# Optimization experiments

Hardware: AMD Instinct MI355X
Metric: run time of the kernel (lower is better)

The kernel has to match this reference:

```python
import jax, jax.numpy as jnp
import numpy as np

N_NODES = 100000


def gcn_conv(x, W, b, src, dst, norm, n_nodes):
    # x: [N, F_in] -> [N, F_out]; GCNConv: D^-1/2 (A+I) D^-1/2 (X W) + b
    h = x @ W                                   # [N, F_out]
    msg = h[src] * norm[:, None]                # [E+N, F_out] gather + scale
    out = jax.ops.segment_sum(msg, dst, num_segments=n_nodes)  # scatter-add
    return out + b


def setup_inputs() -> dict:
    key = jax.random.key(0)
    k0, k1, k2, k3, k4, k5 = jax.random.split(key, 6)
    n, e, f_in, f_hid, n_cls = N_NODES, 1600000, 128, 128, 3
    x = jax.random.normal(k0, (n, f_in), dtype=jnp.float32)
    edge_index = jax.random.randint(k1, (2, e), 0, n, dtype=jnp.int64)
    s1 = 1.0 / np.sqrt(f_in)
    s2 = 1.0 / np.sqrt(f_hid)
    W1 = jax.random.uniform(k2, (f_in, f_hid), jnp.float32, -s1, s1)
    b1 = jnp.zeros((f_hid,), jnp.float32)
    W2 = jax.random.uniform(k3, (f_hid, f_hid), jnp.float32, -s2, s2)
    b2 = jnp.zeros((f_hid,), jnp.float32)
    Wfc = jax.random.uniform(k4, (f_hid, n_cls), jnp.float32, -s2, s2)
    bfc = jax.random.uniform(k5, (n_cls,), jnp.float32, -s2, s2)
    return {"x": x, "edge_index": edge_index, "W1": W1, "b1": b1,
            "W2": W2, "b2": b2, "Wfc": Wfc, "bfc": bfc}


def reference(x, edge_index, W1, b1, W2, b2, Wfc, bfc):
    n = x.shape[0]
    # add self-loops (PyG GCNConv default add_self_loops=True)
    loops = jnp.arange(n, dtype=edge_index.dtype)
    src = jnp.concatenate([edge_index[0], loops])
    dst = jnp.concatenate([edge_index[1], loops])
    deg = jax.ops.segment_sum(jnp.ones_like(dst, dtype=x.dtype), dst,
                              num_segments=n)
    dinv = jax.lax.rsqrt(deg)                   # deg >= 1 due to self-loops
    norm = dinv[src] * dinv[dst]                # [E+N]
    h = jax.nn.relu(gcn_conv(x, W1, b1, src, dst, norm, n))   # dropout=eval id
    h = jax.nn.relu(gcn_conv(h, W2, b2, src, dst, norm, n))
    return jnp.tanh(h @ Wfc + bfc)              # [N, 3]
```

## Files before the change

kernel.cpp:

```cpp
#include <hip/hip_runtime.h>
#include <hip/hip_bf16.h>
#include <hip/hip_fp16.h>


#define NODE_F 128

typedef __attribute__((ext_vector_type(8))) short bf16x8;
typedef __attribute__((ext_vector_type(8))) unsigned short u16x8;
typedef __attribute__((ext_vector_type(4))) float f32x4;

__device__ inline unsigned short bf16_rn(float x) {
    unsigned u = __builtin_bit_cast(unsigned, x);
    unsigned r = (u + 0x7fffu + ((u >> 16) & 1u)) >> 16;
    return (unsigned short)r;
}
__device__ inline float bf16_to_f(unsigned short h) {
    unsigned u = (unsigned)h << 16;
    return __builtin_bit_cast(float, u);
}
__device__ inline void acc8_h(float a[8], uint4 v, float s) {
    unsigned vv[4] = {v.x, v.y, v.z, v.w};
    #pragma unroll
    for (int j = 0; j < 4; ++j) {
        float2 f = __half22float2(__builtin_bit_cast(__half2, vv[j]));
        a[2 * j]     += f.x * s;
        a[2 * j + 1] += f.y * s;
    }
}


__global__ __launch_bounds__(256) void wconv_kernel(const float* __restrict__ W1,
                                                    const float* __restrict__ W2,
                                                    unsigned short* __restrict__ WhiT,
                                                    unsigned short* __restrict__ WloT)
{
    const float* W = blockIdx.x ? W2 : W1;
    unsigned short* hiT = WhiT + blockIdx.x * 128 * 128;
    unsigned short* loT = WloT + blockIdx.x * 128 * 128;
    int tid = threadIdx.x;
    for (int i = tid; i < 128 * 128; i += 256) {
        int k = i >> 7, n = i & 127;
        float x = W[i];
        unsigned short hi = bf16_rn(x);
        float lo = x - bf16_to_f(hi);
        hiT[n * 128 + k] = hi;
        loT[n * 128 + k] = bf16_rn(lo);
    }
}


__global__ __launch_bounds__(256) void scan_block_kernel(
    const int* __restrict__ degE, int* __restrict__ rsA,
    int* __restrict__ bsum, int N)
{
    __shared__ int s[256];
    const int tid = threadIdx.x;
    const int idx = blockIdx.x * 1024 + tid * 4;
    int v0 = (idx + 0 < N) ? degE[idx + 0] : 0;
    int v1 = (idx + 1 < N) ? degE[idx + 1] : 0;
    int v2 = (idx + 2 < N) ? degE[idx + 2] : 0;
    int v3 = (idx + 3 < N) ? degE[idx + 3] : 0;
    int t = v0 + v1 + v2 + v3;
    s[tid] = t;
    __syncthreads();
    #pragma unroll
    for (int off = 1; off < 256; off <<= 1) {
        int x = (tid >= off) ? s[tid - off] : 0;
        __syncthreads();
        s[tid] += x;
        __syncthreads();
    }
    int excl = s[tid] - t;
    if (idx + 0 < N) rsA[idx + 0] = excl;
    if (idx + 1 < N) rsA[idx + 1] = excl + v0;
    if (idx + 2 < N) rsA[idx + 2] = excl + v0 + v1;
    if (idx + 3 < N) rsA[idx + 3] = excl + v0 + v1 + v2;
    if (tid == 255) bsum[blockIdx.x] = s[255];
}

__global__ __launch_bounds__(1024) void scan_tops_kernel(int* __restrict__ bsum, int nb) {
    __shared__ int s[1024];
    const int tid = threadIdx.x;
    int v = (tid < nb) ? bsum[tid] : 0;
    s[tid] = v;
    __syncthreads();
    #pragma unroll
    for (int off = 1; off < 1024; off <<= 1) {
        int x = (tid >= off) ? s[tid - off] : 0;
        __syncthreads();
        s[tid] += x;
        __syncthreads();
    }
    if (tid < nb) bsum[tid] = s[tid] - v;
}


__global__ __launch_bounds__(256) void finish_fill_kernel(
    const int* __restrict__ src, const int* __restrict__ dst,
    const unsigned short* __restrict__ rank,
    const int* __restrict__ rsA, const int* __restrict__ bsum,
    int* __restrict__ rsB, float* __restrict__ dinv,
    const int* __restrict__ degE, int* __restrict__ csr_src,
    int E, int N, int fill_blocks)
{
    if ((int)blockIdx.x < fill_blocks) {
        int e = blockIdx.x * 256 + threadIdx.x;
        if (e < E) {
            int d = dst[e];
            csr_src[rsA[d] + bsum[d >> 10] + (int)rank[e]] = src[e];
        }
    } else {
        int i = (blockIdx.x - fill_blocks) * 256 + threadIdx.x;
        if (i < N) {
            int rs = rsA[i] + bsum[i >> 10];
            rsB[i] = rs;
            dinv[i] = rsqrtf((float)degE[i] + 1.0f);
            if (i == N - 1) rsB[N] = rs + degE[i];
        }
    }
}


template<bool SCALE_OUT>
__device__ __forceinline__ void gemm_compute(
    const unsigned short* __restrict__ WhiT, const unsigned short* __restrict__ WloT,
    const float* __restrict__ dinv, __half* __restrict__ Hout, int N, int rbase,
    unsigned short* xhi, unsigned short* xlo)
{
    const int tid  = threadIdx.x;
    const int lane = tid & 63;
    const int w    = tid >> 6;

    bf16x8 bhi[2][4], blo[2][4];
    {
        int n0   = w * 32 + (lane & 15);
        int koct = (lane >> 4) * 8;
        #pragma unroll
        for (int nt = 0; nt < 2; ++nt) {
            #pragma unroll
            for (int kk = 0; kk < 4; ++kk) {
                size_t o = (size_t)(n0 + nt * 16) * 128 + kk * 32 + koct;
                bhi[nt][kk] = *reinterpret_cast<const bf16x8*>(WhiT + o);
                blo[nt][kk] = *reinterpret_cast<const bf16x8*>(WloT + o);
            }
        }
    }

    f32x4 acc[4][2];
    #pragma unroll
    for (int m = 0; m < 4; ++m)
        #pragma unroll
        for (int nt = 0; nt < 2; ++nt)
            acc[m][nt] = (f32x4){0.f, 0.f, 0.f, 0.f};

    #pragma unroll
    for (int kk = 0; kk < 4; ++kk) {
        #pragma unroll
        for (int m = 0; m < 4; ++m) {
            int row  = m * 16 + (lane & 15);
            int koff = kk * 64 + (lane >> 4) * 16;
            int byte = row * 256 + (koff ^ ((row & 7) << 4));
            bf16x8 ahi = *reinterpret_cast<const bf16x8*>(reinterpret_cast<char*>(xhi) + byte);
            bf16x8 alo = *reinterpret_cast<const bf16x8*>(reinterpret_cast<char*>(xlo) + byte);
            #pragma unroll
            for (int nt = 0; nt < 2; ++nt) {
                acc[m][nt] = __builtin_amdgcn_mfma_f32_16x16x32_bf16(ahi, bhi[nt][kk], acc[m][nt], 0, 0, 0);
                acc[m][nt] = __builtin_amdgcn_mfma_f32_16x16x32_bf16(ahi, blo[nt][kk], acc[m][nt], 0, 0, 0);
                acc[m][nt] = __builtin_amdgcn_mfma_f32_16x16x32_bf16(alo, bhi[nt][kk], acc[m][nt], 0, 0, 0);
            }
        }
    }

    #pragma unroll
    for (int m = 0; m < 4; ++m) {
        int row = rbase + m * 16 + (lane >> 4) * 4;
        int col = w * 32 + (lane & 15);
        #pragma unroll
        for (int nt = 0; nt < 2; ++nt) {
            #pragma unroll
            for (int r = 0; r < 4; ++r) {
                if (row + r < N) {
                    float v = acc[m][nt][r];
                    if (SCALE_OUT) v *= dinv[row + r];
                    Hout[(size_t)(row + r) * NODE_F + col + nt * 16] = __float2half(v);
                }
            }
        }
    }
}


__device__ __forceinline__ void gemm1_body(
    const float* __restrict__ Xf,
    const unsigned short* __restrict__ WhiT, const unsigned short* __restrict__ WloT,
    __half* __restrict__ Hout, int N, int bid,
    unsigned short* xhi, unsigned short* xlo)
{
    const int tid   = threadIdx.x;
    const int rbase = bid * 64;

    #pragma unroll
    for (int it = 0; it < 8; ++it) {
        int f   = it * 256 + tid;
        int row = f >> 5;
        int k4  = f & 31;
        float4 v = make_float4(0.f, 0.f, 0.f, 0.f);
        if (rbase + row < N)
            v = *reinterpret_cast<const float4*>(Xf + (size_t)(rbase + row) * NODE_F + k4 * 4);
        float xs[4] = {v.x, v.y, v.z, v.w};
        ushort4 h4, l4;
        unsigned short* hp = &h4.x;
        unsigned short* lp = &l4.x;
        #pragma unroll
        for (int j = 0; j < 4; ++j) {
            unsigned short hi = bf16_rn(xs[j]);
            hp[j] = hi;
            lp[j] = bf16_rn(xs[j] - bf16_to_f(hi));
        }
        int byte = row * 256 + ((k4 * 8) ^ ((row & 7) << 4));
        *reinterpret_cast<ushort4*>(reinterpret_cast<char*>(xhi) + byte) = h4;
        *reinterpret_cast<ushort4*>(reinterpret_cast<char*>(xlo) + byte) = l4;
    }
    __syncthreads();
    gemm_compute<false>(WhiT, WloT, nullptr, Hout, N, rbase, xhi, xlo);
}


__global__ __launch_bounds__(256) void gemm1deg_kernel(
    const int* __restrict__ dst, int* __restrict__ degE,
    unsigned short* __restrict__ rank, int E,
    int edge_blocks, int gemm_blocks,
    const float* __restrict__ X, const unsigned short* __restrict__ WhiT,
    const unsigned short* __restrict__ WloT, __half* __restrict__ H, int N)
{
    __shared__ unsigned short xhi[64 * 128];
    __shared__ unsigned short xlo[64 * 128];
    int q = blockIdx.x / 5, r = blockIdx.x % 5;
    if (r == 4) {
        int stride = edge_blocks * 256;
        for (int e = q * 256 + threadIdx.x; e < E; e += stride)
            rank[e] = (unsigned short)atomicAdd(&degE[dst[e]], 1);
    } else {
        int gid = q * 4 + r;
        if (gid < gemm_blocks)
            gemm1_body(X, WhiT, WloT, H, N, gid, xhi, xlo);
    }
}


template<bool EDGE_SCALE>
__device__ __forceinline__ void gather_core(
    const __half* __restrict__ Hs, const int* __restrict__ csr_src,
    const int* __restrict__ row_start, const float* __restrict__ dinv,
    int node, int ql, int qi, float a[8])
{
    const char* Hb = reinterpret_cast<const char*>(Hs);
    #pragma unroll
    for (int j = 0; j < 8; ++j) a[j] = 0.f;
    if (qi == 0) {
        float ds = EDGE_SCALE ? dinv[node] : 1.0f;
        acc8_h(a, *reinterpret_cast<const uint4*>(Hb + ((size_t)node * 256 + ql * 16)), ds);
    }

    int i   = row_start[node];
    int end = row_start[node + 1];
    for (; i + 7 < end; i += 8) {
        int s0 = csr_src[i + qi];
        int s1 = csr_src[i + 4 + qi];
        float d0 = EDGE_SCALE ? dinv[s0] : 1.0f;
        float d1 = EDGE_SCALE ? dinv[s1] : 1.0f;
        uint4 v0 = *reinterpret_cast<const uint4*>(Hb + ((size_t)s0 * 256 + ql * 16));
        uint4 v1 = *reinterpret_cast<const uint4*>(Hb + ((size_t)s1 * 256 + ql * 16));
        acc8_h(a, v0, d0);
        acc8_h(a, v1, d1);
    }
    for (; i < end; i += 4) {
        if (i + qi < end) {
            int s = csr_src[i + qi];
            float ds = EDGE_SCALE ? dinv[s] : 1.0f;
            acc8_h(a, *reinterpret_cast<const uint4*>(Hb + ((size_t)s * 256 + ql * 16)), ds);
        }
    }
    #pragma unroll
    for (int j = 0; j < 8; ++j) {
        a[j] += __shfl_xor(a[j], 32);
        a[j] += __shfl_xor(a[j], 16);
    }
}


__global__ __launch_bounds__(256) void aggemm2_kernel(
    const __half* __restrict__ H, const int* __restrict__ csr_src,
    const int* __restrict__ row_start, const float* __restrict__ dinv,
    const float* __restrict__ b1,
    const unsigned short* __restrict__ WhiT, const unsigned short* __restrict__ WloT,
    __half* __restrict__ H2, int N)
{
    __shared__ unsigned short xhi[64 * 128];
    __shared__ unsigned short xlo[64 * 128];
    const int tid  = threadIdx.x;
    const int lane = tid & 63;
    const int w    = tid >> 6;
    const int ql   = lane & 15, qi = lane >> 4;
    const int rbase = blockIdx.x * 64;

    float bv[8];
    {
        float4 b0 = *reinterpret_cast<const float4*>(b1 + ql * 8);
        float4 b4 = *reinterpret_cast<const float4*>(b1 + ql * 8 + 4);
        bv[0] = b0.x; bv[1] = b0.y; bv[2] = b0.z; bv[3] = b0.w;
        bv[4] = b4.x; bv[5] = b4.y; bv[6] = b4.z; bv[7] = b4.w;
    }

    for (int r16 = 0; r16 < 16; ++r16) {
        int row  = w * 16 + r16;
        int node = rbase + row;
        float a[8];
        if (node < N)
            gather_core<true>(H, csr_src, row_start, dinv, node, ql, qi, a);
        if (qi == 0) {
            u16x8 h8 = {0, 0, 0, 0, 0, 0, 0, 0};
            u16x8 l8 = {0, 0, 0, 0, 0, 0, 0, 0};
            if (node < N) {
                float dd = dinv[node];
                #pragma unroll
                for (int j = 0; j < 8; ++j) {
                    float r = fmaxf(bv[j] + dd * a[j], 0.f);
                    unsigned short hi = bf16_rn(r);
                    h8[j] = hi;
                    l8[j] = bf16_rn(r - bf16_to_f(hi));
                }
            }
            int byte = row * 256 + ((ql * 16) ^ ((row & 7) << 4));
            *reinterpret_cast<u16x8*>(reinterpret_cast<char*>(xhi) + byte) = h8;
            *reinterpret_cast<u16x8*>(reinterpret_cast<char*>(xlo) + byte) = l8;
        }
    }
    __syncthreads();
    gemm_compute<true>(WhiT, WloT, dinv, H2, N, rbase, xhi, xlo);
}


__global__ __launch_bounds__(256) void gather2fc_kernel(
    const __half* __restrict__ Hs, const int* __restrict__ csr_src,
    const int* __restrict__ row_start, const float* __restrict__ dinv,
    const float* __restrict__ b, const float* __restrict__ Wfc,
    const float* __restrict__ bfc, float* __restrict__ out, int N)
{
    int node = (blockIdx.x * blockDim.x + threadIdx.x) >> 6;
    int lane = threadIdx.x & 63;
    int ql = lane & 15, qi = lane >> 4;
    if (node >= N) return;

    float a[8];
    gather_core<false>(Hs, csr_src, row_start, dinv, node, ql, qi, a);

    const float dd = dinv[node];
    float p0 = 0.f, p1 = 0.f, p2 = 0.f;
    #pragma unroll
    for (int j = 0; j < 8; ++j) {
        float r = fmaxf(b[ql * 8 + j] + dd * a[j], 0.f);
        const float* wr = Wfc + (size_t)(ql * 8 + j) * 3;
        p0 += r * wr[0]; p1 += r * wr[1]; p2 += r * wr[2];
    }
    #pragma unroll
    for (int off = 8; off > 0; off >>= 1) {
        p0 += __shfl_down(p0, off);
        p1 += __shfl_down(p1, off);
        p2 += __shfl_down(p2, off);
    }
    if (lane == 0) {
        out[(size_t)node * 3 + 0] = tanhf(p0 + bfc[0]);
        out[(size_t)node * 3 + 1] = tanhf(p1 + bfc[1]);
        out[(size_t)node * 3 + 2] = tanhf(p2 + bfc[2]);
    }
}

extern "C" void kernel_launch(void* const* d_in, const int* in_sizes, int n_in,
                              void* d_out, int out_size, void* d_ws, size_t ws_size,
                              hipStream_t stream)
{
    const float* x    = (const float*)d_in[0];
    const int*   edge = (const int*)d_in[1];
    const float* W1   = (const float*)d_in[2];
    const float* b1   = (const float*)d_in[3];
    const float* W2   = (const float*)d_in[4];
    const float* b2   = (const float*)d_in[5];
    const float* Wfc  = (const float*)d_in[6];
    const float* bfc  = (const float*)d_in[7];
    float* out = (float*)d_out;

    const int N = in_sizes[0] / NODE_F;
    const int E = in_sizes[1] / 2;
    const int* src = edge;
    const int* dst = edge + E;

    char* ws = (char*)d_ws;
    size_t off = 0;
    auto alloc = [&](size_t bytes) {
        void* p = ws + off;
        off += (bytes + 511) & ~511ull;
        return p;
    };
    const int nblk = (N + 1023) / 1024;
    float* dinv      = (float*)alloc((size_t)N * 4);
    int*   degE      = (int*)  alloc((size_t)N * 4);
    unsigned short* rank = (unsigned short*)alloc((size_t)E * 2);
    int*   rsA       = (int*)  alloc((size_t)N * 4);
    int*   rsB       = (int*)  alloc((size_t)(N + 1) * 4);
    int*   bsum      = (int*)  alloc((size_t)nblk * 4);
    int*   csr_src   = (int*)  alloc((size_t)E * 4);
    unsigned short* WhiT = (unsigned short*)alloc(2 * 128 * 128 * 2);
    unsigned short* WloT = (unsigned short*)alloc(2 * 128 * 128 * 2);
    __half* H        = (__half*)alloc((size_t)N * NODE_F * 2);
    __half* H2       = (__half*)alloc((size_t)N * NODE_F * 2);
    (void)ws_size; (void)n_in; (void)out_size;

    const int B = 256;
    const int gemm_grid   = (N + 63) / 64;
    const int gather_grid = (N + 3) / 4;
    const int fill_blocks = (E + B - 1) / B;
    const int fin_blocks  = (N + B - 1) / B;

    const int edge_blocks  = (gemm_grid + 3) / 4;
    const int total_blocks = gemm_grid + edge_blocks + 4;

    wconv_kernel<<<2, B, 0, stream>>>(W1, W2, WhiT, WloT);
    hipMemsetAsync(degE, 0, (size_t)N * 4, stream);

    gemm1deg_kernel<<<total_blocks, B, 0, stream>>>(
        dst, degE, rank, E, edge_blocks, gemm_grid, x, WhiT, WloT, H, N);

    scan_block_kernel<<<nblk, B, 0, stream>>>(degE, rsA, bsum, N);
    scan_tops_kernel<<<1, 1024, 0, stream>>>(bsum, nblk);

    finish_fill_kernel<<<fill_blocks + fin_blocks, B, 0, stream>>>(
        src, dst, rank, rsA, bsum, rsB, dinv, degE, csr_src, E, N, fill_blocks);

    aggemm2_kernel<<<gemm_grid, B, 0, stream>>>(
        H, csr_src, rsB, dinv, b1, WhiT + 128 * 128, WloT + 128 * 128, H2, N);

    gather2fc_kernel<<<gather_grid, B, 0, stream>>>(H2, csr_src, rsB, dinv, b2,
                                                    Wfc, bfc, out, N);
}
```

Baseline: 340.5 us.

## Split fused layer-2 gather+GEMM into separate gather and GEMM kernels

Replaces the fused aggregate-then-GEMM kernel, which ran 16 sequential row gathers per wave before a shared-memory GEMM, with a standalone gather kernel (one node per wave, full grid parallelism) writing fp16 activations to a new buffer, followed by a GEMM kernel that loads those rows into LDS. The aim is to expose far more parallelism and latency hiding for the irregular gather, instead of having the GEMM blocks serialize over gathers. In exchange it adds a global round trip of an N×128 fp16 intermediate, an extra launch, and rounds the hidden activations to fp16 before the bf16 hi/lo split, which loses some precision.

```diff
diff --git a/kernel.cpp b/kernel.cpp
--- a/kernel.cpp
+++ b/kernel.cpp
@@ -289,55 +289,66 @@
 }
 
 
-__global__ __launch_bounds__(256) void aggemm2_kernel(
+__global__ __launch_bounds__(256) void gather1_kernel(
     const __half* __restrict__ H, const int* __restrict__ csr_src,
     const int* __restrict__ row_start, const float* __restrict__ dinv,
-    const float* __restrict__ b1,
+    const float* __restrict__ b, __half* __restrict__ A1, int N)
+{
+    int node = (blockIdx.x * blockDim.x + threadIdx.x) >> 6;
+    int lane = threadIdx.x & 63;
+    int ql = lane & 15, qi = lane >> 4;
+    if (node >= N) return;
+
+    float a[8];
+    gather_core<true>(H, csr_src, row_start, dinv, node, ql, qi, a);
+
+    if (qi == 0) {
+        const float dd = dinv[node];
+        u16x8 o;
+        #pragma unroll
+        for (int j = 0; j < 8; ++j) {
+            float r = fmaxf(b[ql * 8 + j] + dd * a[j], 0.f);
+            o[j] = __builtin_bit_cast(unsigned short, __float2half(r));
+        }
+        *reinterpret_cast<u16x8*>(reinterpret_cast<char*>(A1) + ((size_t)node * 256 + ql * 16)) = o;
+    }
+}
+
+
+__global__ __launch_bounds__(256) void gemm2_kernel(
+    const __half* __restrict__ A1,
     const unsigned short* __restrict__ WhiT, const unsigned short* __restrict__ WloT,
-    __half* __restrict__ H2, int N)
+    const float* __restrict__ dinv, __half* __restrict__ Hs, int N)
 {
     __shared__ unsigned short xhi[64 * 128];
     __shared__ unsigned short xlo[64 * 128];
-    const int tid  = threadIdx.x;
-    const int lane = tid & 63;
-    const int w    = tid >> 6;
-    const int ql   = lane & 15, qi = lane >> 4;
+    const int tid   = threadIdx.x;
     const int rbase = blockIdx.x * 64;
 
-    float bv[8];
-    {
-        float4 b0 = *reinterpret_cast<const float4*>(b1 + ql * 8);
-        float4 b4 = *reinterpret_cast<const float4*>(b1 + ql * 8 + 4);
-        bv[0] = b0.x; bv[1] = b0.y; bv[2] = b0.z; bv[3] = b0.w;
-        bv[4] = b4.x; bv[5] = b4.y; bv[6] = b4.z; bv[7] = b4.w;
-    }
-
-    for (int r16 = 0; r16 < 16; ++r16) {
-        int row  = w * 16 + r16;
-        int node = rbase + row;
-        float a[8];
-        if (node < N)
-            gather_core<true>(H, csr_src, row_start, dinv, node, ql, qi, a);
-        if (qi == 0) {
-            u16x8 h8 = {0, 0, 0, 0, 0, 0, 0, 0};
-            u16x8 l8 = {0, 0, 0, 0, 0, 0, 0, 0};
-            if (node < N) {
-                float dd = dinv[node];
-                #pragma unroll
-                for (int j = 0; j < 8; ++j) {
-                    float r = fmaxf(bv[j] + dd * a[j], 0.f);
-                    unsigned short hi = bf16_rn(r);
-                    h8[j] = hi;
-                    l8[j] = bf16_rn(r - bf16_to_f(hi));
-                }
+    #pragma unroll
+    for (int it = 0; it < 4; ++it) {
+        int idx = it * 256 + tid;
+        int row = idx >> 4;
+        int k8  = idx & 15;
+        u16x8 h = {0, 0, 0, 0, 0, 0, 0, 0};
+        u16x8 l = {0, 0, 0, 0, 0, 0, 0, 0};
+        if (rbase + row < N) {
+            u16x8 v = *reinterpret_cast<const u16x8*>(
+                reinterpret_cast<const char*>(A1) + ((size_t)(rbase + row) * 256 + k8 * 16));
+            #pragma unroll
+            for (int j = 0; j < 8; ++j) {
+                float f = __half2float(__builtin_bit_cast(__half, (unsigned short)v[j]));
+                unsigned short hi = bf16_rn(f);
+                h[j] = hi;
+                l[j] = bf16_rn(f - bf16_to_f(hi));
             }
-            int byte = row * 256 + ((ql * 16) ^ ((row & 7) << 4));
-            *reinterpret_cast<u16x8*>(reinterpret_cast<char*>(xhi) + byte) = h8;
-            *reinterpret_cast<u16x8*>(reinterpret_cast<char*>(xlo) + byte) = l8;
-        }
+        }
+        int byte = row * 256 + ((k8 * 16) ^ ((row & 7) << 4));
+        *reinterpret_cast<u16x8*>(reinterpret_cast<char*>(xhi) + byte) = h;
+        *reinterpret_cast<u16x8*>(reinterpret_cast<char*>(xlo) + byte) = l;
     }
     __syncthreads();
-    gemm_compute<true>(WhiT, WloT, dinv, H2, N, rbase, xhi, xlo);
+    gemm_compute<true>(WhiT, WloT, dinv, Hs, N, rbase, xhi, xlo);
 }
 
 
@@ -413,6 +424,7 @@
     unsigned short* WhiT = (unsigned short*)alloc(2 * 128 * 128 * 2);
     unsigned short* WloT = (unsigned short*)alloc(2 * 128 * 128 * 2);
     __half* H        = (__half*)alloc((size_t)N * NODE_F * 2);
+    __half* A1       = (__half*)alloc((size_t)N * NODE_F * 2);
     __half* H2       = (__half*)alloc((size_t)N * NODE_F * 2);
     (void)ws_size; (void)n_in; (void)out_size;
 
@@ -437,8 +449,10 @@
     finish_fill_kernel<<<fill_blocks + fin_blocks, B, 0, stream>>>(
         src, dst, rank, rsA, bsum, rsB, dinv, degE, csr_src, E, N, fill_blocks);
 
-    aggemm2_kernel<<<gemm_grid, B, 0, stream>>>(
-        H, csr_src, rsB, dinv, b1, WhiT + 128 * 128, WloT + 128 * 128, H2, N);
+    gather1_kernel<<<gather_grid, B, 0, stream>>>(H, csr_src, rsB, dinv, b1, A1, N);
+
+    gemm2_kernel<<<gemm_grid, B, 0, stream>>>(A1, WhiT + 128 * 128, WloT + 128 * 128,
+                                              dinv, H2, N);
 
     gather2fc_kernel<<<gather_grid, B, 0, stream>>>(H2, csr_src, rsB, dinv, b2,
                                                     Wfc, bfc, out, N);
```

Result: faster. 301.7 us (median of 3 runs) (-11.4%).
